# Optimization experiments

Hardware: AMD Instinct MI355X
Metric: run time of the kernel (lower is better)

## Reference

```python
import jax, jax.numpy as jnp
import numpy as np

B, H, S, D = 2, 16, 2048, 128

def setup_inputs() -> dict:
    key = jax.random.key(0)
    k1, k2, k3, k4 = jax.random.split(key, 4)
    queries = jax.random.normal(k1, (B, H, S, D), dtype=jnp.float32)
    keys = jax.random.normal(k2, (B, H, S, D), dtype=jnp.float32)
    values = jax.random.normal(k3, (B, H, S, D), dtype=jnp.float32)
    mask = jax.random.randint(k4, (B, 1, S, S), 0, 2).astype(jnp.int32)
    return {"queries": queries, "keys": keys, "values": values, "d_k": D, "mask": mask}

def reference(queries, keys, values, d_k, mask):
    # scores: [B, H, S, S]
    scale = 1.0 / jnp.sqrt(jnp.float32(d_k))
    scores = jnp.einsum('bhqd,bhkd->bhqk', queries, keys) * scale
    if mask is not None:
        scores = scores + (-1e9) * mask.astype(scores.dtype)
    weights = jax.nn.softmax(scores, axis=-1)
    out = jnp.einsum('bhqk,bhkd->bhqd', weights, values)
    return out
```

## Files before the change

### kernel.cpp

```cpp
#include <hip/hip_runtime.h>
#include <hip/hip_bf16.h>

#define BB 2
#define HH 16
#define SS 2048
#define DD 128
#define QBLK 128
#define KVBLK 64
#define NT (SS / KVBLK)
#define TILE_ELEMS (KVBLK * DD)

typedef __bf16 bf16x8 __attribute__((ext_vector_type(8)));
typedef float  f32x16 __attribute__((ext_vector_type(16)));

#define EXP2(x) __builtin_amdgcn_exp2f(x)

__global__ __launch_bounds__(256)
void kimg_prep(const float* __restrict__ K, __bf16* __restrict__ Kd)
{
    #pragma unroll
    for (int i = 0; i < 4; ++i) {
        const int g   = blockIdx.x * 1024 + i * 256 + threadIdx.x;
        const int row = g >> 4;
        const int u   = (g & 15) ^ (row & 7);
        const float* src = K + (size_t)row * 128 + u * 8;
        float4 f0 = *(const float4*)src;
        float4 f1 = *(const float4*)(src + 4);
        bf16x8 h;
        h[0]=(__bf16)f0.x; h[1]=(__bf16)f0.y; h[2]=(__bf16)f0.z; h[3]=(__bf16)f0.w;
        h[4]=(__bf16)f1.x; h[5]=(__bf16)f1.y; h[6]=(__bf16)f1.z; h[7]=(__bf16)f1.w;
        *(bf16x8*)(Kd + (size_t)g * 8) = h;
    }
}

__global__ __launch_bounds__(256)
void vimg_prep(const float* __restrict__ V, __bf16* __restrict__ Vd)
{
    const int g    = blockIdx.x * 256 + threadIdx.x;
    const int tile = g >> 10;
    const int wu   = g & 1023;
    const int d    = wu >> 3;
    const int iu   = wu & 7;
    const int us   = iu ^ (d & 7);
    const int c    = us >> 1;
    const int hh   = us & 1;
    const float* src = V + ((size_t)tile * 64 + c * 16 + 4 * hh) * 128 + d;
    bf16x8 o;
    #pragma unroll
    for (int j = 0; j < 8; ++j) {
        const int roff = (j & 3) + 8 * (j >> 2);
        o[j] = (__bf16)src[(size_t)roff * 128];
    }
    *(bf16x8*)(Vd + (size_t)g * 8) = o;
}

__global__ __launch_bounds__(256)
void mprep(const int* __restrict__ M, unsigned* __restrict__ mb)
{
    const int wid  = blockIdx.x * 4 + (threadIdx.x >> 6);
    const int lane = threadIdx.x & 63;
    const int kb   = wid & 31;
    const int q    = (wid >> 5) & 2047;
    const int b    = wid >> 16;
    const int mi   = M[((size_t)b * 2048 + q) * 2048 + kb * 64 + lane];
    const unsigned long long bal = __ballot(mi != 0);
    if (lane == 0) {
        uint2 st; st.x = (unsigned)bal; st.y = (unsigned)(bal >> 32);
        *(uint2*)&mb[((size_t)b * 2048 + q) * 64 + kb * 2] = st;
    }
}

__device__ __forceinline__ void load_lds16(const __bf16* g, __bf16* l) {
    __builtin_amdgcn_global_load_lds(
        (const __attribute__((address_space(1))) void*)g,
        (__attribute__((address_space(3))) void*)l, 16, 0, 0);
}

#define WAIT_VM(N)                                                             \
    do {                                                                       \
        asm volatile("s_waitcnt vmcnt(" #N ")" ::: "memory");                  \
        __builtin_amdgcn_sched_barrier(0);                                     \
    } while (0)

#define BAR() __builtin_amdgcn_s_barrier()

#define ISSUE_LDS(BUF)                                                         \
    do {                                                                       \
        _Pragma("unroll")                                                      \
        for (int i = 0; i < 4; ++i)                                            \
            load_lds16(kgp + i * 512, SM + (BUF) * 8192 + w * 2048 + i * 512); \
        _Pragma("unroll")                                                      \
        for (int i = 0; i < 4; ++i)                                            \
            load_lds16(vgp + i * 512, SM + 16384 + (BUF) * 8192 + w * 2048 + i * 512); \
        kgp += TILE_ELEMS;                                                     \
        vgp += TILE_ELEMS;                                                     \
    } while (0)

#define ISSUE_M(MST)                                                           \
    do { MST = *(const uint2*)mp; mp += 2; } while (0)

#define COMPUTE_TILE(BUF, MST)                                                 \
    do {                                                                       \
        f32x16 s[2];                                                           \
        __builtin_amdgcn_s_setprio(1);                                         \
        _Pragma("unroll")                                                      \
        for (int ko = 0; ko < 2; ++ko) {                                       \
            s[ko] = (f32x16)0.0f;                                              \
            _Pragma("unroll")                                                  \
            for (int d0 = 0; d0 < 8; ++d0) {                                   \
                bf16x8 kf = *(const bf16x8*)(kp[d0] + (BUF) * 8192 + ko * 4096); \
                s[ko] = __builtin_amdgcn_mfma_f32_32x32x16_bf16(kf, qf[d0], s[ko], 0, 0, 0); \
            }                                                                  \
        }                                                                      \
        __builtin_amdgcn_s_setprio(0);                                         \
        float mx = s[0][0];                                                    \
        _Pragma("unroll")                                                      \
        for (int ko = 0; ko < 2; ++ko)                                         \
            _Pragma("unroll")                                                  \
            for (int j = (ko ? 0 : 1); j < 16; ++j) mx = fmaxf(mx, s[ko][j]);  \
        mx = fmaxf(mx, __shfl_xor(mx, 32));                                    \
        if (__any(mx > m2 + 11.5415603f)) {       \
            const float newm  = fmaxf(m2, mx);                                 \
            const float alpha = EXP2(m2 - newm);                               \
            m2 = newm;                                                         \
            l_i *= alpha;                                                      \
            _Pragma("unroll")                                                  \
            for (int dd = 0; dd < 4; ++dd)                                     \
                _Pragma("unroll")                                              \
                for (int j = 0; j < 16; ++j) o[dd][j] *= alpha;                \
        }                                                                      \
        float rs = 0.0f;                                                       \
        {                                                                      \
            const unsigned mw0 = (MST.x) >> sh4;                               \
            const unsigned mw1 = (MST.y) >> sh4;                               \
            _Pragma("unroll")                                                  \
            for (int j = 0; j < 16; ++j) {                                     \
                const unsigned bit = 1u << ((j & 3) + 8 * (j >> 2));           \
                float p0 = EXP2(s[0][j] - m2); p0 = (mw0 & bit) ? 0.0f : p0;   \
                float p1 = EXP2(s[1][j] - m2); p1 = (mw1 & bit) ? 0.0f : p1;   \
                s[0][j] = p0; s[1][j] = p1;                                    \
                rs += p0 + p1;                                                 \
            }                                                                  \
        }                                                                      \
        rs += __shfl_xor(rs, 32);                                              \
        l_i += rs;                                                             \
        __builtin_amdgcn_s_setprio(1);                                         \
        _Pragma("unroll")                                                      \
        for (int c = 0; c < 4; ++c) {                                          \
            const int ko = c >> 1, cc = c & 1;                                 \
            bf16x8 pb;                                                         \
            _Pragma("unroll")                                                  \
            for (int r = 0; r < 8; ++r) pb[r] = (__bf16)s[ko][cc * 8 + r];     \
            _Pragma("unroll")                                                  \
            for (int dd = 0; dd < 4; ++dd) {                                   \
                bf16x8 va = *(const bf16x8*)(vp[c] + (BUF) * 8192 + dd * 2048); \
                o[dd] = __builtin_amdgcn_mfma_f32_32x32x16_bf16(va, pb, o[dd], 0, 0, 0); \
            }                                                                  \
        }                                                                      \
        __builtin_amdgcn_s_setprio(0);                                         \
    } while (0)

#define HALF_ITER(BUF, MREG)                                                   \
    do {                                                                       \
        COMPUTE_TILE(BUF, MREG);                                               \
        BAR();                                                                 \
        ISSUE_LDS(BUF);                                                        \
        ISSUE_M(MREG);                                                         \
        WAIT_VM(9);                                                            \
        BAR();                                                                 \
    } while (0)

__global__ __launch_bounds__(256, 2)
void attn_fwd(const float* __restrict__ Q, const __bf16* __restrict__ Kimg,
              const __bf16* __restrict__ Vimg, const unsigned* __restrict__ MB,
              float* __restrict__ O)
{
    __shared__ __bf16 SM[4 * TILE_ELEMS];

    const int tid  = threadIdx.x;
    const int lane = tid & 63;
    const int ln31 = lane & 31;
    const int h    = lane >> 5;
    const int sw   = lane & 7;
    const int w    = tid >> 6;
    const int sh4  = 4 * h;

    const int bid = blockIdx.x;
    const int swz = (bid & 7) * 64 + (bid >> 3);
    const int qb  = swz & 15;
    const int bh  = swz >> 4;
    const int b   = bh >> 4;

    const float SC = 0.08838834764831845f * 1.4426950408889634f;

    const float* Qb = Q + (size_t)bh * SS * DD;
    float*       Ob = O + (size_t)bh * SS * DD;

    const int qrow = qb * QBLK + w * 32 + ln31;

    const __bf16*   kgp = Kimg + (size_t)bh * SS * DD + w * 2048 + lane * 8;
    const __bf16*   vgp = Vimg + (size_t)bh * SS * DD + w * 2048 + lane * 8;
    const unsigned* mp  = MB + ((size_t)b * 2048 + qrow) * 64;

    const __bf16* kp[8];
    const __bf16* vp[4];
    #pragma unroll
    for (int j = 0; j < 8; ++j)
        kp[j] = SM + ln31 * 128 + (((j * 2 + h) ^ sw) * 8);
    #pragma unroll
    for (int j = 0; j < 4; ++j)
        vp[j] = SM + 16384 + ln31 * 64 + (((j * 2 + h) ^ sw) * 8);

    bf16x8 qf[8];
    {
        const float* qr = Qb + (size_t)qrow * DD + 8 * h;
        #pragma unroll
        for (int d0 = 0; d0 < 8; ++d0) {
            float4 f0 = *(const float4*)(qr + d0 * 16);
            float4 f1 = *(const float4*)(qr + d0 * 16 + 4);
            bf16x8 a;
            a[0]=(__bf16)(f0.x*SC); a[1]=(__bf16)(f0.y*SC);
            a[2]=(__bf16)(f0.z*SC); a[3]=(__bf16)(f0.w*SC);
            a[4]=(__bf16)(f1.x*SC); a[5]=(__bf16)(f1.y*SC);
            a[6]=(__bf16)(f1.z*SC); a[7]=(__bf16)(f1.w*SC);
            qf[d0] = a;
        }
    }
    __builtin_amdgcn_sched_barrier(0);

    f32x16 o[4];
    #pragma unroll
    for (int i = 0; i < 4; ++i) o[i] = (f32x16)0.0f;
    float m2 = -1e30f, l_i = 0.0f;

    uint2 mA, mB2;

    ISSUE_LDS(0);
    ISSUE_M(mA);
    ISSUE_LDS(1);
    ISSUE_M(mB2);
    WAIT_VM(9);
    BAR();

    #pragma unroll 1
    for (int t = 0; t + 3 < NT; t += 2) {
        HALF_ITER(0, mA);
        HALF_ITER(1, mB2);
    }
    COMPUTE_TILE(0, mA);
    WAIT_VM(0);
    BAR();
    COMPUTE_TILE(1, mB2);

    const float inv = 1.0f / l_i;
    float* orow = Ob + (size_t)qrow * DD + 4 * h;
    #pragma unroll
    for (int dd = 0; dd < 4; ++dd) {
        #pragma unroll
        for (int rg = 0; rg < 4; ++rg) {
            float4 st;
            st.x = o[dd][rg*4+0] * inv; st.y = o[dd][rg*4+1] * inv;
            st.z = o[dd][rg*4+2] * inv; st.w = o[dd][rg*4+3] * inv;
            *(float4*)&orow[dd * 32 + rg * 8] = st;
        }
    }
}

extern "C" void kernel_launch(void* const* d_in, const int* in_sizes, int n_in,
                              void* d_out, int out_size, void* d_ws, size_t ws_size,
                              hipStream_t stream) {
    const float* Q = (const float*)d_in[0];
    const float* K = (const float*)d_in[1];
    const float* V = (const float*)d_in[2];
    const int*   M = (const int*)d_in[4];
    float*       O = (float*)d_out;

    __bf16*   Kimg = (__bf16*)d_ws;
    __bf16*   Vimg = Kimg + (size_t)BB * HH * SS * DD;
    unsigned* Mbit = (unsigned*)(Vimg + (size_t)BB * HH * SS * DD);

    kimg_prep<<<1024, 256, 0, stream>>>(K, Kimg);
    vimg_prep<<<4096, 256, 0, stream>>>(V, Vimg);
    mprep    <<<32768, 256, 0, stream>>>(M, Mbit);

    attn_fwd<<<BB * HH * (SS / QBLK), 256, 0, stream>>>(Q, Kimg, Vimg, Mbit, O);
}
```

Before: 131.9 us.

## Split KV range across two blocks and merge partials in a combine kernel

Splits each attention block's key range into two halves, giving twice as many workgroups (1024) with smaller KV tiles of 32. It raises the occupancy target to 4 blocks per SIMD and reworks the K/V LDS swizzles and the V image prep, which now uses an LDS transpose. Each half writes a bf16 partial output plus its running max and sum, and a new combine kernel merges them into fp32. The aim is better GPU fill and latency hiding, at the cost of extra partial-output traffic, another launch, and bf16 rounding of the partials.

```diff
diff --git a/kernel.cpp b/kernel.cpp
--- a/kernel.cpp
+++ b/kernel.cpp
@@ -6,11 +6,13 @@
 #define SS 2048
 #define DD 128
 #define QBLK 128
-#define KVBLK 64
-#define NT (SS / KVBLK)
+#define KVBLK 32
+#define NTB 32
 #define TILE_ELEMS (KVBLK * DD)
+#define NROWS (BB * HH * SS)
 
 typedef __bf16 bf16x8 __attribute__((ext_vector_type(8)));
+typedef __bf16 bf16x4 __attribute__((ext_vector_type(4)));
 typedef float  f32x16 __attribute__((ext_vector_type(16)));
 
 #define EXP2(x) __builtin_amdgcn_exp2f(x)
@@ -22,7 +24,7 @@
     for (int i = 0; i < 4; ++i) {
         const int g   = blockIdx.x * 1024 + i * 256 + threadIdx.x;
         const int row = g >> 4;
-        const int u   = (g & 15) ^ (row & 7);
+        const int u   = (g & 15) ^ (row & 15);
         const float* src = K + (size_t)row * 128 + u * 8;
         float4 f0 = *(const float4*)src;
         float4 f1 = *(const float4*)(src + 4);
@@ -36,22 +38,29 @@
 __global__ __launch_bounds__(256)
 void vimg_prep(const float* __restrict__ V, __bf16* __restrict__ Vd)
 {
-    const int g    = blockIdx.x * 256 + threadIdx.x;
-    const int tile = g >> 10;
-    const int wu   = g & 1023;
-    const int d    = wu >> 3;
-    const int iu   = wu & 7;
-    const int us   = iu ^ (d & 7);
-    const int c    = us >> 1;
-    const int hh   = us & 1;
-    const float* src = V + ((size_t)tile * 64 + c * 16 + 4 * hh) * 128 + d;
-    bf16x8 o;
-    #pragma unroll
-    for (int j = 0; j < 8; ++j) {
-        const int roff = (j & 3) + 8 * (j >> 2);
-        o[j] = (__bf16)src[(size_t)roff * 128];
-    }
-    *(bf16x8*)(Vd + (size_t)g * 8) = o;
+    __shared__ float T[KVBLK][DD + 1];
+    const int tile = blockIdx.x;
+    const float* src = V + (size_t)tile * KVBLK * DD;
+    #pragma unroll
+    for (int i = 0; i < 4; ++i) {
+        const int slot = i * 256 + threadIdx.x;
+        const int k = slot >> 5, c4 = slot & 31;
+        float4 f = *(const float4*)(src + (size_t)k * DD + c4 * 4);
+        T[k][c4*4+0] = f.x; T[k][c4*4+1] = f.y;
+        T[k][c4*4+2] = f.z; T[k][c4*4+3] = f.w;
+    }
+    __syncthreads();
+    #pragma unroll
+    for (int i = 0; i < 4; ++i) {
+        const int gu = i * 256 + threadIdx.x;
+        const int d  = gu >> 3;
+        const int j  = (gu & 7) ^ ((d >> 1) & 7);
+        const int kb = (j >> 2) * 16 + ((j >> 1) & 1) * 4 + (j & 1) * 8;
+        bf16x4 o;
+        o[0] = (__bf16)T[kb+0][d]; o[1] = (__bf16)T[kb+1][d];
+        o[2] = (__bf16)T[kb+2][d]; o[3] = (__bf16)T[kb+3][d];
+        *(bf16x4*)(Vd + (size_t)tile * TILE_ELEMS + (size_t)gu * 4) = o;
+    }
 }
 
 __global__ __launch_bounds__(256)
@@ -86,38 +95,31 @@
 
 #define ISSUE_LDS(BUF)                                                         \
     do {                                                                       \
-        _Pragma("unroll")                                                      \
-        for (int i = 0; i < 4; ++i)                                            \
-            load_lds16(kgp + i * 512, SM + (BUF) * 8192 + w * 2048 + i * 512); \
-        _Pragma("unroll")                                                      \
-        for (int i = 0; i < 4; ++i)                                            \
-            load_lds16(vgp + i * 512, SM + 16384 + (BUF) * 8192 + w * 2048 + i * 512); \
+        load_lds16(kgp,       SM + (BUF) * 4096 + w * 1024);                   \
+        load_lds16(kgp + 512, SM + (BUF) * 4096 + w * 1024 + 512);             \
+        load_lds16(vgp,       SM + 8192 + (BUF) * 4096 + w * 1024);            \
+        load_lds16(vgp + 512, SM + 8192 + (BUF) * 4096 + w * 1024 + 512);      \
         kgp += TILE_ELEMS;                                                     \
         vgp += TILE_ELEMS;                                                     \
     } while (0)
 
 #define ISSUE_M(MST)                                                           \
-    do { MST = *(const uint2*)mp; mp += 2; } while (0)
+    do { MST = *mp; mp += 1; } while (0)
 
 #define COMPUTE_TILE(BUF, MST)                                                 \
     do {                                                                       \
-        f32x16 s[2];                                                           \
+        f32x16 s = (f32x16)0.0f;                                               \
         __builtin_amdgcn_s_setprio(1);                                         \
         _Pragma("unroll")                                                      \
-        for (int ko = 0; ko < 2; ++ko) {                                       \
-            s[ko] = (f32x16)0.0f;                                              \
-            _Pragma("unroll")                                                  \
-            for (int d0 = 0; d0 < 8; ++d0) {                                   \
-                bf16x8 kf = *(const bf16x8*)(kp[d0] + (BUF) * 8192 + ko * 4096); \
-                s[ko] = __builtin_amdgcn_mfma_f32_32x32x16_bf16(kf, qf[d0], s[ko], 0, 0, 0); \
-            }                                                                  \
+        for (int d0 = 0; d0 < 8; ++d0) {                                       \
+            bf16x8 kf = *(const bf16x8*)(kp[d0] + (BUF) * 4096);               \
+            s = __builtin_amdgcn_mfma_f32_32x32x16_bf16(kf, qf[d0], s, 0, 0, 0); \
         }                                                                      \
         __builtin_amdgcn_s_setprio(0);                                         \
-        float mx = s[0][0];                                                    \
-        _Pragma("unroll")                                                      \
-        for (int ko = 0; ko < 2; ++ko)                                         \
-            _Pragma("unroll")                                                  \
-            for (int j = (ko ? 0 : 1); j < 16; ++j) mx = fmaxf(mx, s[ko][j]);  \
+        float mx = fmaxf(fmaxf(fmaxf(s[0], s[1]), fmaxf(s[2], s[3])),          \
+                         fmaxf(fmaxf(s[4], s[5]), fmaxf(s[6], s[7])));         \
+        mx = fmaxf(mx, fmaxf(fmaxf(fmaxf(s[8], s[9]), fmaxf(s[10], s[11])),    \
+                             fmaxf(fmaxf(s[12], s[13]), fmaxf(s[14], s[15])))); \
         mx = fmaxf(mx, __shfl_xor(mx, 32));                                    \
         if (__any(mx > m2 + 11.5415603f)) {       \
             const float newm  = fmaxf(m2, mx);                                 \
@@ -130,34 +132,29 @@
                 for (int j = 0; j < 16; ++j) o[dd][j] *= alpha;                \
         }                                                                      \
         float rs = 0.0f;                                                       \
-        {                                                                      \
-            const unsigned mw0 = (MST.x) >> sh4;                               \
-            const unsigned mw1 = (MST.y) >> sh4;                               \
+        _Pragma("unroll")                                                      \
+        for (int c = 0; c < 2; ++c) {        \
+            const unsigned wc = MST >> (16 * c + sh4);                         \
+            bf16x8 pb;                                                         \
             _Pragma("unroll")                                                  \
-            for (int j = 0; j < 16; ++j) {                                     \
-                const unsigned bit = 1u << ((j & 3) + 8 * (j >> 2));           \
-                float p0 = EXP2(s[0][j] - m2); p0 = (mw0 & bit) ? 0.0f : p0;   \
-                float p1 = EXP2(s[1][j] - m2); p1 = (mw1 & bit) ? 0.0f : p1;   \
-                s[0][j] = p0; s[1][j] = p1;                                    \
-                rs += p0 + p1;                                                 \
+            for (int r = 0; r < 8; ++r) {                                      \
+                float p = EXP2(s[c * 8 + r] - m2);                             \
+                p = (wc & (1u << ((r & 3) + 8 * (r >> 2)))) ? 0.0f : p;        \
+                rs += p;                                                       \
+                pb[r] = (__bf16)p;                                             \
             }                                                                  \
+            __builtin_amdgcn_s_setprio(1);                                     \
+            _Pragma("unroll")                                                  \
+            for (int dd = 0; dd < 4; ++dd) {                                   \
+                bf16x4 lo = *(const bf16x4*)(vp[c * 2]     + (BUF) * 4096 + dd * 1024); \
+                bf16x4 hi = *(const bf16x4*)(vp[c * 2 + 1] + (BUF) * 4096 + dd * 1024); \
+                bf16x8 va = __builtin_shufflevector(lo, hi, 0, 1, 2, 3, 4, 5, 6, 7); \
+                o[dd] = __builtin_amdgcn_mfma_f32_32x32x16_bf16(va, pb, o[dd], 0, 0, 0); \
+            }                                                                  \
+            __builtin_amdgcn_s_setprio(0);                                     \
         }                                                                      \
         rs += __shfl_xor(rs, 32);                                              \
         l_i += rs;                                                             \
-        __builtin_amdgcn_s_setprio(1);                                         \
-        _Pragma("unroll")                                                      \
-        for (int c = 0; c < 4; ++c) {                                          \
-            const int ko = c >> 1, cc = c & 1;                                 \
-            bf16x8 pb;                                                         \
-            _Pragma("unroll")                                                  \
-            for (int r = 0; r < 8; ++r) pb[r] = (__bf16)s[ko][cc * 8 + r];     \
-            _Pragma("unroll")                                                  \
-            for (int dd = 0; dd < 4; ++dd) {                                   \
-                bf16x8 va = *(const bf16x8*)(vp[c] + (BUF) * 8192 + dd * 2048); \
-                o[dd] = __builtin_amdgcn_mfma_f32_32x32x16_bf16(va, pb, o[dd], 0, 0, 0); \
-            }                                                                  \
-        }                                                                      \
-        __builtin_amdgcn_s_setprio(0);                                         \
     } while (0)
 
 #define HALF_ITER(BUF, MREG)                                                   \
@@ -166,14 +163,14 @@
         BAR();                                                                 \
         ISSUE_LDS(BUF);                                                        \
         ISSUE_M(MREG);                                                         \
-        WAIT_VM(9);                                                            \
+        WAIT_VM(5);                                                            \
         BAR();                                                                 \
     } while (0)
 
-__global__ __launch_bounds__(256, 2)
+__global__ __launch_bounds__(256, 4)
 void attn_fwd(const float* __restrict__ Q, const __bf16* __restrict__ Kimg,
               const __bf16* __restrict__ Vimg, const unsigned* __restrict__ MB,
-              float* __restrict__ O)
+              __bf16* __restrict__ OP, float2* __restrict__ ML)
 {
     __shared__ __bf16 SM[4 * TILE_ELEMS];
 
@@ -181,35 +178,38 @@
     const int lane = tid & 63;
     const int ln31 = lane & 31;
     const int h    = lane >> 5;
-    const int sw   = lane & 7;
     const int w    = tid >> 6;
     const int sh4  = 4 * h;
 
     const int bid = blockIdx.x;
-    const int swz = (bid & 7) * 64 + (bid >> 3);
-    const int qb  = swz & 15;
-    const int bh  = swz >> 4;
+    const int swz = (bid & 7) * 128 + (bid >> 3);
+    const int kh  = swz >> 9;
+    const int rem = swz & 511;
+    const int qb  = rem & 15;
+    const int bh  = rem >> 4;
     const int b   = bh >> 4;
 
     const float SC = 0.08838834764831845f * 1.4426950408889634f;
 
     const float* Qb = Q + (size_t)bh * SS * DD;
-    float*       Ob = O + (size_t)bh * SS * DD;
-
     const int qrow = qb * QBLK + w * 32 + ln31;
 
-    const __bf16*   kgp = Kimg + (size_t)bh * SS * DD + w * 2048 + lane * 8;
-    const __bf16*   vgp = Vimg + (size_t)bh * SS * DD + w * 2048 + lane * 8;
-    const unsigned* mp  = MB + ((size_t)b * 2048 + qrow) * 64;
-
+    const __bf16*   kgp = Kimg + ((size_t)bh * SS + kh * 1024) * DD + w * 1024 + lane * 8;
+    const __bf16*   vgp = Vimg + ((size_t)bh * 64 + kh * 32) * TILE_ELEMS + w * 1024 + lane * 8;
+    const unsigned* mp  = MB + ((size_t)b * 2048 + qrow) * 64 + kh * 32;
+
+    const int kkey = ln31 & 15;
+    const int vkey = (ln31 >> 1) & 7;
     const __bf16* kp[8];
+    #pragma unroll
+    for (int d0 = 0; d0 < 8; ++d0)
+        kp[d0] = SM + ln31 * 128 + (((2 * d0 + h) ^ kkey) * 8);
     const __bf16* vp[4];
     #pragma unroll
-    for (int j = 0; j < 8; ++j)
-        kp[j] = SM + ln31 * 128 + (((j * 2 + h) ^ sw) * 8);
-    #pragma unroll
-    for (int j = 0; j < 4; ++j)
-        vp[j] = SM + 16384 + ln31 * 64 + (((j * 2 + h) ^ sw) * 8);
+    for (int u = 0; u < 4; ++u) {
+        const int c = u >> 1, bb = u & 1;
+        vp[u] = SM + 8192 + ln31 * 32 + (((c * 4 + 2 * h + bb) ^ vkey) * 4);
+    }
 
     bf16x8 qf[8];
     {
@@ -233,17 +233,17 @@
     for (int i = 0; i < 4; ++i) o[i] = (f32x16)0.0f;
     float m2 = -1e30f, l_i = 0.0f;
 
-    uint2 mA, mB2;
+    unsigned mA, mB2;
 
     ISSUE_LDS(0);
     ISSUE_M(mA);
     ISSUE_LDS(1);
     ISSUE_M(mB2);
-    WAIT_VM(9);
+    WAIT_VM(5);
     BAR();
 
     #pragma unroll 1
-    for (int t = 0; t + 3 < NT; t += 2) {
+    for (int t = 0; t + 3 < NTB; t += 2) {
         HALF_ITER(0, mA);
         HALF_ITER(1, mB2);
     }
@@ -252,17 +252,59 @@
     BAR();
     COMPUTE_TILE(1, mB2);
 
-    const float inv = 1.0f / l_i;
-    float* orow = Ob + (size_t)qrow * DD + 4 * h;
+    const float inv = (l_i > 0.0f) ? 1.0f / l_i : 0.0f;
+    __bf16* opr = OP + ((size_t)(kh * 32 + bh) * SS + qrow) * DD;
     #pragma unroll
     for (int dd = 0; dd < 4; ++dd) {
         #pragma unroll
         for (int rg = 0; rg < 4; ++rg) {
-            float4 st;
-            st.x = o[dd][rg*4+0] * inv; st.y = o[dd][rg*4+1] * inv;
-            st.z = o[dd][rg*4+2] * inv; st.w = o[dd][rg*4+3] * inv;
-            *(float4*)&orow[dd * 32 + rg * 8] = st;
+            bf16x4 st;
+            st[0] = (__bf16)(o[dd][rg*4+0] * inv);
+            st[1] = (__bf16)(o[dd][rg*4+1] * inv);
+            st[2] = (__bf16)(o[dd][rg*4+2] * inv);
+            st[3] = (__bf16)(o[dd][rg*4+3] * inv);
+            *(bf16x4*)&opr[dd * 32 + rg * 8 + 4 * h] = st;
         }
+    }
+    if (h == 0) {
+        float2 ml; ml.x = m2; ml.y = l_i;
+        ML[(size_t)(kh * 32 + bh) * SS + qrow] = ml;
+    }
+}
+
+__global__ __launch_bounds__(256)
+void combine(const __bf16* __restrict__ OP, const float2* __restrict__ ML,
+             float* __restrict__ O)
+{
+    const int gid = blockIdx.x * 256 + threadIdx.x;
+    const int row = gid >> 3;
+    const int dc  = gid & 7;
+    const float2 ml0 = ML[row];
+    const float2 ml1 = ML[(size_t)NROWS + row];
+    const float  M   = fmaxf(ml0.x, ml1.x);
+    const float  w0  = (ml0.y > 0.0f) ? EXP2(ml0.x - M) * ml0.y : 0.0f;
+    const float  w1  = (ml1.y > 0.0f) ? EXP2(ml1.x - M) * ml1.y : 0.0f;
+    const float  inv = 1.0f / (w0 + w1);
+    const float  c0 = w0 * inv, c1 = w1 * inv;
+
+    const __bf16* p0 = OP + (size_t)row * DD + dc * 16;
+    const __bf16* p1 = p0 + (size_t)NROWS * DD;
+    bf16x8 a0 = *(const bf16x8*)p0;
+    bf16x8 b0 = *(const bf16x8*)(p0 + 8);
+    bf16x8 a1 = *(const bf16x8*)p1;
+    bf16x8 b1 = *(const bf16x8*)(p1 + 8);
+
+    float* op = O + (size_t)row * DD + dc * 16;
+    float r[16];
+    #pragma unroll
+    for (int j = 0; j < 8; ++j) {
+        r[j]     = c0 * (float)a0[j] + c1 * (float)a1[j];
+        r[j + 8] = c0 * (float)b0[j] + c1 * (float)b1[j];
+    }
+    #pragma unroll
+    for (int q4 = 0; q4 < 4; ++q4) {
+        float4 st; st.x = r[q4*4]; st.y = r[q4*4+1]; st.z = r[q4*4+2]; st.w = r[q4*4+3];
+        *(float4*)&op[q4 * 4] = st;
     }
 }
 
@@ -275,13 +317,17 @@
     const int*   M = (const int*)d_in[4];
     float*       O = (float*)d_out;
 
+    const size_t NE = (size_t)BB * HH * SS * DD;
     __bf16*   Kimg = (__bf16*)d_ws;
-    __bf16*   Vimg = Kimg + (size_t)BB * HH * SS * DD;
-    unsigned* Mbit = (unsigned*)(Vimg + (size_t)BB * HH * SS * DD);
+    __bf16*   Vimg = Kimg + NE;
+    unsigned* Mbit = (unsigned*)(Vimg + NE);
+    __bf16*   OP   = (__bf16*)(Mbit + (size_t)BB * SS * 64);
+    float2*   MLp  = (float2*)(OP + 2 * NE);
 
     kimg_prep<<<1024, 256, 0, stream>>>(K, Kimg);
-    vimg_prep<<<4096, 256, 0, stream>>>(V, Vimg);
+    vimg_prep<<<2048, 256, 0, stream>>>(V, Vimg);
     mprep    <<<32768, 256, 0, stream>>>(M, Mbit);
 
-    attn_fwd<<<BB * HH * (SS / QBLK), 256, 0, stream>>>(Q, Kimg, Vimg, Mbit, O);
-}
+    attn_fwd<<<1024, 256, 0, stream>>>(Q, Kimg, Vimg, Mbit, OP, MLp);
+    combine <<<2048, 256, 0, stream>>>(OP, MLp, O);
+}
```

Result: slower. 259.0 us (+96.3%).
